# Kernel tuning notes

Measured on AMD Instinct MI355X. Metric: run time of the kernel, lower is better.

The kernel has to match this reference:

```python
import jax, jax.numpy as jnp
import numpy as np

P = 10          # num_patches
EPS = 1e-20
ALPHAS = dict(stretch=1.0, E=1.0, G=1.0, skew=1.0, total_area=1.0, total_area_mult=1.0)
ALPHA_MC = 1.0
ALPHA_DISTORT = 1.0


def setup_inputs() -> dict:
    key = jax.random.key(0)
    k1, k2, k3, k4 = jax.random.split(key, 4)
    B, N, M = 8, 8192, 2500
    pc_gt = jax.random.normal(k1, (B, N, 3), dtype=jnp.float32)
    pc_pred = jax.random.normal(k2, (B, M, 3), dtype=jnp.float32)
    # first fundamental form (E, F, G); ensure E*G - F^2 > 0 so sqrt is smooth
    u = jax.random.uniform(k3, (B, M, 3), dtype=jnp.float32)
    fff = u * 0.5 + jnp.array([1.0, 0.0, 1.0], dtype=jnp.float32)
    A_gt = jax.random.uniform(k4, (B,), dtype=jnp.float32)
    return {"pc_gt": pc_gt, "pc_pred": pc_pred, "fff": fff, "A_gt": A_gt}


def _forward(pc_gt, pc_pred, fff, A_gt):
    B, M, _ = pc_pred.shape
    spp = M // P

    # ---- Chamfer distance via dense (B, M, N) distance matrix + argmin ----
    diff = pc_pred[:, :, None, :] - pc_gt[:, None, :, :]          # (B, M, N, 3)
    distm = jnp.sqrt(jnp.sum(diff * diff, axis=3))                # (B, M, N)
    inds_p2gt = jnp.argmin(distm, axis=2)                         # (B, M)
    inds_gt2p = jnp.argmin(distm, axis=1)                         # (B, N)
    pc_gt_reg = jnp.take_along_axis(pc_gt, inds_p2gt[..., None], axis=1)   # (B, M, 3)
    pc_p_reg = jnp.take_along_axis(pc_pred, inds_gt2p[..., None], axis=1)  # (B, N, 3)
    d_p2gt = jnp.sum((pc_pred - pc_gt_reg) ** 2, axis=2)
    d_gt2p = jnp.sum((pc_gt - pc_p_reg) ** 2, axis=2)
    L_chd = d_p2gt.mean() + d_gt2p.mean()

    # ---- FFF-based losses ----
    EFG = jnp.transpose(fff.reshape(B, P, spp, 3), (3, 0, 1, 2))  # (3, B, P, spp)
    E, F, G = EFG[0], EFG[1], EFG[2]

    # metric consistency between consecutive frame pairs
    Eh = E.reshape(B // 2, 2, P, spp)
    Fh = F.reshape(B // 2, 2, P, spp)
    Gh = G.reshape(B // 2, 2, P, spp)
    L_mc = ((Eh[:, 0] - Eh[:, 1]) ** 2
            + 2.0 * (Fh[:, 0] - Fh[:, 1]) ** 2
            + (Gh[:, 0] - Gh[:, 1]) ** 2).mean()

    # scaled isometry (collapse) losses
    A2 = jnp.maximum(E * G - F * F, 0.0)                          # (B, P, spp)
    A = jnp.sqrt(A2)
    inv = 1.0 / (A2 + EPS)
    L_stretch = (((E - G) ** 2) * inv).mean() * ALPHAS['stretch']
    L_E = (((E - E.mean()) ** 2) * inv).mean() * ALPHAS['E']
    L_G = (((G - G.mean()) ** 2) * inv).mean() * ALPHAS['G']
    L_F = ((F * F) * inv).mean() * ALPHAS['skew']

    # overlap / total-area loss
    A_tot = A.mean(axis=2).sum(axis=1)                            # (B,)
    L_olap = (jnp.maximum(0.0, A_tot - A_gt * ALPHAS['total_area_mult']) ** 2).mean() * ALPHAS['total_area']

    loss_sciso = L_F + L_E + L_G + L_stretch + L_olap
    loss_tot = L_chd + ALPHA_MC * L_mc + ALPHA_DISTORT * loss_sciso
    return loss_tot


def reference(pc_gt, pc_pred, fff, A_gt):
    return _forward(pc_gt, pc_pred, fff, A_gt)
```

## Files before the change

### kernel.cpp

```cpp
#include <hip/hip_runtime.h>

#define B_   8
#define N_   8192
#define M_   2500
#define SPP_ 250
#define EPS_ 1e-20f
#define BIGF 1e30f

#define NB_CH   640
#define NB_FFF  79
#define NB_K1   (NB_CH + NB_FFF)

#define NB_SG   64
#define NB_SP   20
#define NB_K2   (NB_SG + NB_SP)

#define WS_P2M  0
#define WS_G2M  20000
#define WS_ACC  85536
#define WS_CNT  (WS_ACC + 20)
#define A_E    0
#define A_G    1
#define A_MC   2
#define A_ST   3
#define A_F2I  4
#define A_E2I  5
#define A_EI   6
#define A_G2I  7
#define A_GI   8
#define A_I    9
#define A_AB   10
#define A_SP   18
#define A_SG   19

typedef __attribute__((ext_vector_type(8))) short short8_t;
typedef __attribute__((ext_vector_type(4))) float float4_t;

__device__ __forceinline__ unsigned pack_bf2(float lo, float hi) {
    unsigned a = __float_as_uint(lo);
    unsigned b = __float_as_uint(hi);
    a = (a + 0x7FFFu + ((a >> 16) & 1u)) >> 16;
    b = (b + 0x7FFFu + ((b >> 16) & 1u)) & 0xFFFF0000u;
    return a | b;
}
__device__ __forceinline__ short bf16s(float x) {
    unsigned a = __float_as_uint(x);
    return (short)((a + 0x7FFFu + ((a >> 16) & 1u)) >> 16);
}
__device__ __forceinline__ float min3f(float a, float b, float c) {
    float r;
    asm("v_min3_f32 %0, %1, %2, %3" : "=v"(r) : "v"(a), "v"(b), "v"(c));
    return r;
}
__device__ __forceinline__ float wave_sum64(float v) {
    #pragma unroll
    for (int o = 32; o > 0; o >>= 1) v += __shfl_down(v, o, 64);
    return v;
}
__device__ __forceinline__ float block_sum256(float v, volatile float* red4) {
    v = wave_sum64(v);
    int wid = threadIdx.x >> 6, lane = threadIdx.x & 63;
    if (lane == 0) red4[wid] = v;
    __syncthreads();
    float r = 0.f;
    if (threadIdx.x == 0) r = red4[0] + red4[1] + red4[2] + red4[3];
    __syncthreads();
    return r;
}
__device__ __forceinline__ void quad_min4(float4_t& c) {
    #pragma unroll
    for (int m = 1; m < 16; m <<= 1) {
        c.x = fminf(c.x, __shfl_xor(c.x, m, 64));
        c.y = fminf(c.y, __shfl_xor(c.y, m, 64));
        c.z = fminf(c.z, __shfl_xor(c.z, m, 64));
        c.w = fminf(c.w, __shfl_xor(c.w, m, 64));
    }
}

__global__ void __launch_bounds__(256, 2) k1_main(
        const float* __restrict__ gt, const float* __restrict__ pred,
        const float* __restrict__ fff, float* __restrict__ ws) {
    __shared__ uint4 spts[512];
    __shared__ __align__(16) float saux[516];
    __shared__ float scol[4][4][520];
    const int bid = blockIdx.x;
    const int tid = threadIdx.x;
    const int lane = tid & 63;
    const int w    = tid >> 6;
    const int quad = lane >> 4;
    const int l15  = lane & 15;
    float* acc = ws + WS_ACC;

    if (bid < NB_CH) {
        const int z = bid / 40;
        const int rem = bid % 40;
        const int b = rem / 5;
        const int mblk = rem % 5;
        const float* apts = pred + (size_t)b * M_ * 3;
        const float* bpts = gt + ((size_t)b * N_ + (size_t)z * 512) * 3;
        const int abase = mblk * 512;
        float* dstR = ws + WS_P2M + (size_t)b * M_;
        float* dstC = ws + WS_G2M + (size_t)b * N_ + z * 512;

        for (int i = tid; i < 512; i += 256) {
            const float* q3 = bpts + i * 3;
            float x = q3[0], y = q3[1], zc = q3[2];
            float n2 = x * x + y * y + zc * zc;
            uint4 q;
            q.x = pack_bf2(-2.f * x, -2.f * y);
            q.y = pack_bf2(-2.f * zc, n2);
            q.z = q.x; q.w = q.y;
            spts[i] = q;
        }

        short8_t af[8];
        #pragma unroll
        for (int t = 0; t < 8; ++t) af[t] = (short8_t){0,0,0,0,0,0,0,0};
        if (lane < 16) {
            #pragma unroll
            for (int t = 0; t < 8; ++t) {
                int m = abase + w * 128 + t * 16 + l15;
                int c = m < M_ ? m : M_ - 1;
                float x = apts[c*3+0], y = apts[c*3+1], zc = apts[c*3+2];
                af[t][0] = bf16s(x); af[t][1] = bf16s(y); af[t][2] = bf16s(zc);
                af[t][3] = (short)0x3F80;
                saux[w * 128 + t * 16 + l15] = x*x + y*y + zc*zc;
            }
        }
        __syncthreads();

        const float4_t* bp = (const float4_t*)saux;
        float4_t bias[8], c[8];
        #pragma unroll
        for (int t = 0; t < 8; ++t) {
            bias[t] = bp[w * 32 + t * 4 + quad];
            c[t] = (float4_t){BIGF, BIGF, BIGF, BIGF};
        }

        const uint4* bptr = spts + l15;
        #pragma unroll 2
        for (int ip = 0; ip < 16; ++ip) {
            short8_t bf0 = __builtin_bit_cast(short8_t, bptr[(2*ip+0) * 16]);
            short8_t bf1 = __builtin_bit_cast(short8_t, bptr[(2*ip+1) * 16]);
            float4_t d0[8], d1[8];
            #pragma unroll
            for (int t = 0; t < 8; ++t)
                d0[t] = __builtin_amdgcn_mfma_f32_16x16x32_bf16(af[t], bf0, bias[t], 0, 0, 0);
            #pragma unroll
            for (int t = 0; t < 8; ++t)
                d1[t] = __builtin_amdgcn_mfma_f32_16x16x32_bf16(af[t], bf1, bias[t], 0, 0, 0);
            float cA0 = BIGF, cB0 = BIGF, cA1 = BIGF, cB1 = BIGF;
            #pragma unroll
            for (int t = 0; t < 8; ++t) {
                c[t].x = min3f(c[t].x, d0[t].x, d1[t].x);
                c[t].y = min3f(c[t].y, d0[t].y, d1[t].y);
                c[t].z = min3f(c[t].z, d0[t].z, d1[t].z);
                c[t].w = min3f(c[t].w, d0[t].w, d1[t].w);
                float m0 = min3f(d0[t].x, d0[t].y, d0[t].z);
                float m1 = min3f(d1[t].x, d1[t].y, d1[t].z);
                if (t & 1) { cB0 = min3f(cB0, m0, d0[t].w); cB1 = min3f(cB1, m1, d1[t].w); }
                else       { cA0 = min3f(cA0, m0, d0[t].w); cA1 = min3f(cA1, m1, d1[t].w); }
            }
            scol[w][quad][(2*ip+0)*16 + l15] = fminf(cA0, cB0);
            scol[w][quad][(2*ip+1)*16 + l15] = fminf(cA1, cB1);
        }

        #pragma unroll
        for (int t = 0; t < 8; ++t) {
            quad_min4(c[t]);
            if (l15 == 0) {
                int m0 = abase + w * 128 + t * 16 + quad * 4;
                if (m0 < M_) {
                    atomicMin((int*)(dstR + m0 + 0), (int)__float_as_uint(fmaxf(c[t].x, 0.f)));
                    atomicMin((int*)(dstR + m0 + 1), (int)__float_as_uint(fmaxf(c[t].y, 0.f)));
                    atomicMin((int*)(dstR + m0 + 2), (int)__float_as_uint(fmaxf(c[t].z, 0.f)));
                    atomicMin((int*)(dstR + m0 + 3), (int)__float_as_uint(fmaxf(c[t].w, 0.f)));
                }
            }
        }

        __syncthreads();
        #pragma unroll
        for (int rr = 0; rr < 2; ++rr) {
            int j = rr * 256 + tid;
            float v = BIGF;
            #pragma unroll
            for (int w2 = 0; w2 < 4; ++w2)
                #pragma unroll
                for (int q = 0; q < 4; ++q)
                    v = fminf(v, scol[w2][q][j]);
            atomicMin((int*)(dstC + j), (int)__float_as_uint(fmaxf(v, 0.f)));
        }
    } else {
        const int kb = bid - NB_CH;
        const int i  = kb * 256 + tid;
        volatile float* red4 = saux + 512;
        float* sA = saux;
        if (tid < B_) sA[tid] = 0.f;
        __syncthreads();

        float vE=0.f,vG=0.f,vMC=0.f,vST=0.f,vF2=0.f,vE2=0.f,vEI=0.f,
              vG2=0.f,vGI=0.f,vI=0.f;
        if (i < B_ * M_) {
            const int b = i / M_;
            const int m = i - b * M_;
            const float* f = fff + (size_t)i * 3;
            float E = f[0], F = f[1], G = f[2];
            float A2  = fmaxf(E * G - F * F, 0.f);
            float inv = 1.f / (A2 + EPS_);
            vE = E; vG = G;
            vST = (E - G) * (E - G) * inv;
            vF2 = F * F * inv;
            vE2 = E * E * inv; vEI = E * inv;
            vG2 = G * G * inv; vGI = G * inv;
            vI  = inv;
            atomicAdd(&sA[b], sqrtf(A2));
            if ((b & 1) == 0) {
                const float* f2 = fff + ((size_t)(b + 1) * M_ + m) * 3;
                float dE = E - f2[0], dF = F - f2[1], dG = G - f2[2];
                vMC = dE * dE + 2.f * dF * dF + dG * dG;
            }
        }
        float r;
        r = block_sum256(vE,  red4); if (tid==0) atomicAdd(&acc[A_E],   r);
        r = block_sum256(vG,  red4); if (tid==0) atomicAdd(&acc[A_G],   r);
        r = block_sum256(vMC, red4); if (tid==0) atomicAdd(&acc[A_MC],  r);
        r = block_sum256(vST, red4); if (tid==0) atomicAdd(&acc[A_ST],  r);
        r = block_sum256(vF2, red4); if (tid==0) atomicAdd(&acc[A_F2I], r);
        r = block_sum256(vE2, red4); if (tid==0) atomicAdd(&acc[A_E2I], r);
        r = block_sum256(vEI, red4); if (tid==0) atomicAdd(&acc[A_EI],  r);
        r = block_sum256(vG2, red4); if (tid==0) atomicAdd(&acc[A_G2I], r);
        r = block_sum256(vGI, red4); if (tid==0) atomicAdd(&acc[A_GI],  r);
        r = block_sum256(vI,  red4); if (tid==0) atomicAdd(&acc[A_I],   r);
        __syncthreads();
        if (tid < B_ && sA[tid] != 0.f) atomicAdd(&acc[A_AB + tid], sA[tid]);
    }
}

__global__ void __launch_bounds__(256) k2_reduce(
        const float* __restrict__ fff, const float* __restrict__ A_gt,
        float* __restrict__ ws, float* __restrict__ out) {
    __shared__ float red4[4];
    const int bid = blockIdx.x;
    const int tid = threadIdx.x;
    float* acc = ws + WS_ACC;

    if (bid < NB_SG) {
        const float* src = ws + WS_G2M + (size_t)bid * 1024;
        float s = 0.f;
        #pragma unroll
        for (int j = 0; j < 4; ++j) s += src[tid + j * 256];
        float r = block_sum256(s, red4);
        if (tid == 0) atomicAdd(&acc[A_SG], r);
    } else {
        const int kb = bid - NB_SG;
        float s = 0.f;
        #pragma unroll
        for (int j = 0; j < 4; ++j) {
            int o = kb * 1024 + tid + j * 256;
            if (o < 20000) s += ws[WS_P2M + o];
        }
        float r = block_sum256(s, red4);
        if (tid == 0) atomicAdd(&acc[A_SP], r);
    }

    __syncthreads();
    if (tid == 0) __threadfence();
    __syncthreads();
    __shared__ unsigned old_s;
    if (tid == 0)
        old_s = __hip_atomic_fetch_add((unsigned*)(ws + WS_CNT), 1u,
                                       __ATOMIC_ACQ_REL, __HIP_MEMORY_SCOPE_AGENT);
    __syncthreads();
    if (old_s == (unsigned)(NB_K2 - 1) && tid == 0) {
        float a[20];
        #pragma unroll
        for (int k = 0; k < 20; ++k)
            a[k] = __hip_atomic_load(&acc[k], __ATOMIC_RELAXED,
                                     __HIP_MEMORY_SCOPE_AGENT);
        const float inv20k = 1.f / 20000.f;
        float mE = a[A_E] * inv20k, mG = a[A_G] * inv20k;
        float L_E = (a[A_E2I] - 2.f*mE*a[A_EI] + mE*mE*a[A_I]) * inv20k;
        float L_G = (a[A_G2I] - 2.f*mG*a[A_GI] + mG*mG*a[A_I]) * inv20k;
        float L_sc = L_E + L_G + (a[A_ST] + a[A_F2I]) * inv20k;
        float L_mc = a[A_MC] * (1.f / 10000.f);
        float L_chd = a[A_SP] * inv20k + a[A_SG] * (1.f / 65536.f);
        float L_olap = 0.f;
        #pragma unroll
        for (int b = 0; b < B_; ++b) {
            float At = a[A_AB + b] * (1.f / (float)SPP_);
            float d  = fmaxf(0.f, At - A_gt[b]);
            L_olap += d * d;
        }
        L_olap *= (1.f / (float)B_);
        out[0] = L_chd + L_mc + L_sc + L_olap;
    }
}

extern "C" void kernel_launch(void* const* d_in, const int* in_sizes, int n_in,
                              void* d_out, int out_size, void* d_ws, size_t ws_size,
                              hipStream_t stream) {
    const float* pc_gt   = (const float*)d_in[0];
    const float* pc_pred = (const float*)d_in[1];
    const float* fff     = (const float*)d_in[2];
    const float* A_gt    = (const float*)d_in[3];
    float* ws  = (float*)d_ws;
    float* out = (float*)d_out;

    hipMemsetAsync(ws, 0x7F, (size_t)WS_ACC * sizeof(float), stream);
    hipMemsetAsync(ws + WS_ACC, 0, 21 * sizeof(float), stream);
    k1_main  <<<NB_K1, 256, 0, stream>>>(pc_gt, pc_pred, fff, ws);
    k2_reduce<<<NB_K2, 256, 0, stream>>>(fff, A_gt, ws, out);
}
```

Baseline: 91.47 us.

## Fuse final reduction into main kernel via last-block counter, drop second launch

Removes the separate reduction kernel and one memset. The last block of the main kernel, found with an atomic counter that starts from the 0x7F memset pattern, now sums the per-point Chamfer minima and the per-block FFF partials. FFF blocks write their partial sums to dedicated slots instead of using float atomics. The aim is to save a launch and the extra memset, at the cost of a single block doing the whole final ~85K-element reduction serially.

```diff
diff --git a/kernel.cpp b/kernel.cpp
--- a/kernel.cpp
+++ b/kernel.cpp
@@ -9,16 +9,13 @@
 
 #define NB_CH   640
 #define NB_FFF  79
-#define NB_K1   (NB_CH + NB_FFF)
-
-#define NB_SG   64
-#define NB_SP   20
-#define NB_K2   (NB_SG + NB_SP)
+#define NB_TOT  (NB_CH + NB_FFF)
+#define CNT_INIT 0x7F7F7F7Fu
 
 #define WS_P2M  0
 #define WS_G2M  20000
-#define WS_ACC  85536
-#define WS_CNT  (WS_ACC + 20)
+#define WS_CNT  85536
+#define WS_SLOT 85540
 #define A_E    0
 #define A_G    1
 #define A_MC   2
@@ -30,8 +27,6 @@
 #define A_GI   8
 #define A_I    9
 #define A_AB   10
-#define A_SP   18
-#define A_SG   19
 
 typedef __attribute__((ext_vector_type(8))) short short8_t;
 typedef __attribute__((ext_vector_type(4))) float float4_t;
@@ -79,17 +74,19 @@
 
 __global__ void __launch_bounds__(256, 2) k1_main(
         const float* __restrict__ gt, const float* __restrict__ pred,
-        const float* __restrict__ fff, float* __restrict__ ws) {
+        const float* __restrict__ fff, const float* __restrict__ A_gt,
+        float* __restrict__ ws, float* __restrict__ out) {
     __shared__ uint4 spts[512];
     __shared__ __align__(16) float saux[516];
     __shared__ float scol[4][4][520];
+    __shared__ unsigned old_s;
     const int bid = blockIdx.x;
     const int tid = threadIdx.x;
     const int lane = tid & 63;
     const int w    = tid >> 6;
     const int quad = lane >> 4;
     const int l15  = lane & 15;
-    float* acc = ws + WS_ACC;
+    volatile float* red4 = saux + 512;
 
     if (bid < NB_CH) {
         const int z = bid / 40;
@@ -194,7 +191,7 @@
     } else {
         const int kb = bid - NB_CH;
         const int i  = kb * 256 + tid;
-        volatile float* red4 = saux + 512;
+        float* slot = ws + WS_SLOT + (size_t)kb * 18;
         float* sA = saux;
         if (tid < B_) sA[tid] = 0.f;
         __syncthreads();
@@ -222,69 +219,61 @@
             }
         }
         float r;
-        r = block_sum256(vE,  red4); if (tid==0) atomicAdd(&acc[A_E],   r);
-        r = block_sum256(vG,  red4); if (tid==0) atomicAdd(&acc[A_G],   r);
-        r = block_sum256(vMC, red4); if (tid==0) atomicAdd(&acc[A_MC],  r);
-        r = block_sum256(vST, red4); if (tid==0) atomicAdd(&acc[A_ST],  r);
-        r = block_sum256(vF2, red4); if (tid==0) atomicAdd(&acc[A_F2I], r);
-        r = block_sum256(vE2, red4); if (tid==0) atomicAdd(&acc[A_E2I], r);
-        r = block_sum256(vEI, red4); if (tid==0) atomicAdd(&acc[A_EI],  r);
-        r = block_sum256(vG2, red4); if (tid==0) atomicAdd(&acc[A_G2I], r);
-        r = block_sum256(vGI, red4); if (tid==0) atomicAdd(&acc[A_GI],  r);
-        r = block_sum256(vI,  red4); if (tid==0) atomicAdd(&acc[A_I],   r);
+        r = block_sum256(vE,  red4); if (tid==0) slot[A_E]   = r;
+        r = block_sum256(vG,  red4); if (tid==0) slot[A_G]   = r;
+        r = block_sum256(vMC, red4); if (tid==0) slot[A_MC]  = r;
+        r = block_sum256(vST, red4); if (tid==0) slot[A_ST]  = r;
+        r = block_sum256(vF2, red4); if (tid==0) slot[A_F2I] = r;
+        r = block_sum256(vE2, red4); if (tid==0) slot[A_E2I] = r;
+        r = block_sum256(vEI, red4); if (tid==0) slot[A_EI]  = r;
+        r = block_sum256(vG2, red4); if (tid==0) slot[A_G2I] = r;
+        r = block_sum256(vGI, red4); if (tid==0) slot[A_GI]  = r;
+        r = block_sum256(vI,  red4); if (tid==0) slot[A_I]   = r;
         __syncthreads();
-        if (tid < B_ && sA[tid] != 0.f) atomicAdd(&acc[A_AB + tid], sA[tid]);
-    }
-}
-
-__global__ void __launch_bounds__(256) k2_reduce(
-        const float* __restrict__ fff, const float* __restrict__ A_gt,
-        float* __restrict__ ws, float* __restrict__ out) {
-    __shared__ float red4[4];
-    const int bid = blockIdx.x;
-    const int tid = threadIdx.x;
-    float* acc = ws + WS_ACC;
-
-    if (bid < NB_SG) {
-        const float* src = ws + WS_G2M + (size_t)bid * 1024;
-        float s = 0.f;
-        #pragma unroll
-        for (int j = 0; j < 4; ++j) s += src[tid + j * 256];
-        float r = block_sum256(s, red4);
-        if (tid == 0) atomicAdd(&acc[A_SG], r);
-    } else {
-        const int kb = bid - NB_SG;
-        float s = 0.f;
-        #pragma unroll
-        for (int j = 0; j < 4; ++j) {
-            int o = kb * 1024 + tid + j * 256;
-            if (o < 20000) s += ws[WS_P2M + o];
-        }
-        float r = block_sum256(s, red4);
-        if (tid == 0) atomicAdd(&acc[A_SP], r);
+        if (tid < B_) slot[A_AB + tid] = sA[tid];
     }
 
     __syncthreads();
     if (tid == 0) __threadfence();
     __syncthreads();
-    __shared__ unsigned old_s;
     if (tid == 0)
         old_s = __hip_atomic_fetch_add((unsigned*)(ws + WS_CNT), 1u,
                                        __ATOMIC_ACQ_REL, __HIP_MEMORY_SCOPE_AGENT);
     __syncthreads();
-    if (old_s == (unsigned)(NB_K2 - 1) && tid == 0) {
-        float a[20];
-        #pragma unroll
-        for (int k = 0; k < 20; ++k)
-            a[k] = __hip_atomic_load(&acc[k], __ATOMIC_RELAXED,
-                                     __HIP_MEMORY_SCOPE_AGENT);
+    if (old_s != CNT_INIT + (unsigned)(NB_TOT - 1)) return;
+
+    float sP = 0.f;
+    const float4_t* p4 = (const float4_t*)(ws + WS_P2M);
+    for (int i = tid; i < 5000; i += 256) {
+        float4_t v = p4[i];
+        sP += (v.x + v.y) + (v.z + v.w);
+    }
+    float rSP = block_sum256(sP, red4);
+
+    float sG = 0.f;
+    const float4_t* g4 = (const float4_t*)(ws + WS_G2M);
+    #pragma unroll 4
+    for (int i = tid; i < 16384; i += 256) {
+        float4_t v = g4[i];
+        sG += (v.x + v.y) + (v.z + v.w);
+    }
+    float rSG = block_sum256(sG, red4);
+
+    float a[18];
+    #pragma unroll
+    for (int k = 0; k < 18; ++k) {
+        float v = (tid < NB_FFF) ? ws[WS_SLOT + (size_t)tid * 18 + k] : 0.f;
+        a[k] = block_sum256(v, red4);
+    }
+
+    if (tid == 0) {
         const float inv20k = 1.f / 20000.f;
         float mE = a[A_E] * inv20k, mG = a[A_G] * inv20k;
         float L_E = (a[A_E2I] - 2.f*mE*a[A_EI] + mE*mE*a[A_I]) * inv20k;
         float L_G = (a[A_G2I] - 2.f*mG*a[A_GI] + mG*mG*a[A_I]) * inv20k;
         float L_sc = L_E + L_G + (a[A_ST] + a[A_F2I]) * inv20k;
         float L_mc = a[A_MC] * (1.f / 10000.f);
-        float L_chd = a[A_SP] * inv20k + a[A_SG] * (1.f / 65536.f);
+        float L_chd = rSP * inv20k + rSG * (1.f / 65536.f);
         float L_olap = 0.f;
         #pragma unroll
         for (int b = 0; b < B_; ++b) {
@@ -307,8 +296,6 @@
     float* ws  = (float*)d_ws;
     float* out = (float*)d_out;
 
-    hipMemsetAsync(ws, 0x7F, (size_t)WS_ACC * sizeof(float), stream);
-    hipMemsetAsync(ws + WS_ACC, 0, 21 * sizeof(float), stream);
-    k1_main  <<<NB_K1, 256, 0, stream>>>(pc_gt, pc_pred, fff, ws);
-    k2_reduce<<<NB_K2, 256, 0, stream>>>(fff, A_gt, ws, out);
-}
+    hipMemsetAsync(ws, 0x7F, (size_t)(WS_CNT + 4) * sizeof(float), stream);
+    k1_main<<<NB_TOT, 256, 0, stream>>>(pc_gt, pc_pred, fff, A_gt, ws, out);
+}
```

After: 116.9 us. 27.8% more time.
